# Kernel optimization log

Hardware: AMD Instinct MI355X
Metric: run time of the kernel (lower is better)

## Reference

```python
import jax, jax.numpy as jnp
import numpy as np

DEC_H = 1024
ENC_H_TOTAL = 1024  # enc_hid_size * enc_num_dirs


def setup_inputs() -> dict:
    key = jax.random.key(0)
    ks = jax.random.split(key, 10)
    N, L = 64, 1024
    s = 0.02
    return {
        "dec_h_curr": jax.random.normal(ks[0], (N, DEC_H), jnp.float32),
        "enc_hids": jax.random.normal(ks[1], (N, L, ENC_H_TOTAL), jnp.float32),
        # project_dec_hids: Linear(dec_H, dec_H)
        "W_dec": jax.random.normal(ks[2], (DEC_H, DEC_H), jnp.float32) * s,
        "b_dec": jnp.zeros((DEC_H,), jnp.float32),
        # project_enc_hids: Linear(enc_H*nDir, dec_H)
        "W_enc": jax.random.normal(ks[3], (ENC_H_TOTAL, DEC_H), jnp.float32) * s,
        "b_enc": jnp.zeros((DEC_H,), jnp.float32),
        # project_to_one_dim: Linear(dec_H, 1)
        "W_one": jax.random.normal(ks[4], (DEC_H, 1), jnp.float32) * s,
        "b_one": jnp.zeros((1,), jnp.float32),
        # project_att_hids: Linear(enc_H*nDir, dec_H)
        "W_att": jax.random.normal(ks[5], (ENC_H_TOTAL, DEC_H), jnp.float32) * s,
        "b_att": jnp.zeros((DEC_H,), jnp.float32),
    }


def reference(dec_h_curr, enc_hids, W_dec, b_dec, W_enc, b_enc, W_one, b_one, W_att, b_att):
    # additive (Bahdanau) attention branch
    d = dec_h_curr @ W_dec + b_dec                     # N x dec_H
    e = jnp.einsum('nle,ed->nld', enc_hids, W_enc) + b_enc  # N x L x dec_H
    scores = jnp.einsum('nld,do->nl', jnp.tanh(d[:, None, :] + e), W_one) + b_one[0]  # N x L
    alpha = jax.nn.softmax(scores, axis=-1)            # N x L
    ctx = jnp.einsum('nl,nle->ne', alpha, enc_hids)    # N x enc_H_total
    h_att_curr = ctx @ W_att + b_att                   # N x dec_H
    return h_att_curr, alpha
```

## Files before the change

kernel.cpp:

```cpp
#include <hip/hip_runtime.h>
#include <cstdio>
#include <cstdint>


typedef __bf16 bf16x8 __attribute__((ext_vector_type(8)));
typedef float f32x4 __attribute__((ext_vector_type(4)));
typedef unsigned short us8 __attribute__((ext_vector_type(8)));

static __device__ __forceinline__ unsigned short f2b(float f) {
  union { float f; unsigned u; } v; v.f = f;
  unsigned r = (v.u + 0x7fffu + ((v.u >> 16) & 1u)) >> 16;
  return (unsigned short)r;
}
static __device__ __forceinline__ float b2f(unsigned short u) {
  union { unsigned u; float f; } v; v.u = ((unsigned)u) << 16;
  return v.f;
}
static __device__ __forceinline__ void gl_lds16(const void* g, void* l) {
  __builtin_amdgcn_global_load_lds(
      (const __attribute__((address_space(1))) unsigned int*)g,
      (__attribute__((address_space(3))) unsigned int*)l, 16, 0, 0);
}
static __device__ __forceinline__ float fast_tanh(float x) {
  float ax = __builtin_fminf(__builtin_fabsf(x), 18.0f);
  float u = __builtin_amdgcn_exp2f(ax * 2.88539008177792681f);
  float t = (u - 1.0f) * __builtin_amdgcn_rcpf(u + 1.0f);
  return __builtin_copysignf(t, x);
}

__global__ __launch_bounds__(256) void prep_k(
    const float* __restrict__ enc, unsigned short* __restrict__ Ap,
    const float* __restrict__ W_enc, unsigned short* __restrict__ Bp,
    const float* __restrict__ dec_h, const float* __restrict__ W_dec,
    const float* __restrict__ b_dec, const float* __restrict__ b_enc,
    float* __restrict__ addterm) {
  __shared__ __align__(16) unsigned short tile[8192];
  const int bid = blockIdx.x;
  const int t = threadIdx.x;

  if (bid < 128) {
    const int Tn = bid >> 4, kt = bid & 15;
    #pragma unroll
    for (int it = 0; it < 8; ++it) {
      int idx = it * 256 + t;
      int kk = idx >> 5, n4 = idx & 31;
      const float4 v = *(const float4*)(W_enc + (size_t)(kt * 64 + kk) * 1024 + Tn * 128 + n4 * 4);
      int c = kk >> 3, j = kk & 7;
      #pragma unroll
      for (int x = 0; x < 4; ++x) {
        int mm = n4 * 4 + x;
        float fv = (x == 0) ? v.x : (x == 1) ? v.y : (x == 2) ? v.z : v.w;
        tile[(mm * 8 + (c ^ (mm & 7))) * 8 + j] = f2b(fv);
      }
    }
    __syncthreads();
    #pragma unroll
    for (int it = 0; it < 4; ++it) {
      int p = it * 256 + t;
      int c = p >> 7, m = p & 127;
      us8 v = *(const us8*)&tile[(m * 8 + (c ^ (m & 7))) * 8];
      *(us8*)(Bp + ((size_t)bid * 1024 + p) * 8) = v;
    }
  } else if (bid < 384) {
    const int bid2 = bid - 128;
    const int jb = bid2 & 3, n = bid2 >> 2;
    float* xs = (float*)tile;
    for (int i = t; i < 1024; i += 256) xs[i] = dec_h[n * 1024 + i];
    __syncthreads();
    int j = jb * 256 + t;
    float s = 0.f;
    #pragma unroll 8
    for (int k = 0; k < 1024; ++k) s += xs[k] * W_dec[(size_t)k * 1024 + j];
    addterm[n * 1024 + j] = s + b_dec[j] + b_enc[j];
  } else {
    const int ba = bid - 384;
    const int T = ba >> 4, kt = ba & 15;
    #pragma unroll
    for (int it = 0; it < 8; ++it) {
      int idx = it * 256 + t;
      int m = idx >> 4, c4 = idx & 15;
      const float4 v = *(const float4*)(enc + (size_t)(T * 128 + m) * 1024 + kt * 64 + c4 * 4);
      ushort4 o;
      o.x = f2b(v.x); o.y = f2b(v.y); o.z = f2b(v.z); o.w = f2b(v.w);
      int c = c4 >> 1, half = c4 & 1;
      *(ushort4*)&tile[(m * 8 + (c ^ (m & 7))) * 8 + half * 4] = o;
    }
    __syncthreads();
    #pragma unroll
    for (int it = 0; it < 4; ++it) {
      int p = it * 256 + t;
      int c = p >> 7, m = p & 127;
      us8 v = *(const us8*)&tile[(m * 8 + (c ^ (m & 7))) * 8];
      *(us8*)(Ap + ((size_t)ba * 1024 + p) * 8) = v;
    }
  }
}

__global__ __launch_bounds__(512, 2) void score_gemm(
    const unsigned short* __restrict__ Ap, const unsigned short* __restrict__ Bp,
    const float* __restrict__ addterm, const float* __restrict__ Wone,
    float* __restrict__ spart) {
  __shared__ __align__(16) unsigned short lA[32768];
  __shared__ __align__(16) unsigned short lB[32768];
  const int tid = threadIdx.x;
  const int lane = tid & 63, wave = tid >> 6;
  const int wm = wave >> 2, wn = wave & 3;
  const int q = lane >> 4, r = lane & 15;

  const int flat = blockIdx.x;
  const int tl = (flat & 7) * 128 + (flat >> 3);
  const int nb = tl & 3, mb = tl >> 2;

  f32x4 acc[8][4];
  #pragma unroll
  for (int i = 0; i < 8; ++i)
    #pragma unroll
    for (int j = 0; j < 4; ++j) acc[i][j] = (f32x4){0.f, 0.f, 0.f, 0.f};

  const unsigned short* gA0 = Ap + (((size_t)(2 * mb + 0) * 16) * 1024 + tid) * 8;
  const unsigned short* gA1 = Ap + (((size_t)(2 * mb + 1) * 16) * 1024 + tid) * 8;
  const unsigned short* gB0 = Bp + (((size_t)(2 * nb + 0) * 16) * 1024 + tid) * 8;
  const unsigned short* gB1 = Bp + (((size_t)(2 * nb + 1) * 16) * 1024 + tid) * 8;

  const unsigned short* rdA = &lA[(wm * 1024 + q * 128 + r) * 8];
  const unsigned short* rdB = &lB[((wn >> 1) * 1024 + q * 128 + (wn & 1) * 64 + r) * 8];

  bf16x8 af[4], bg[4];

#define SA(h, t, s) gl_lds16((h ? gA1 : gA0) + ((size_t)(t) * 1024 + (s) * 512) * 8, \
                             &lA[((((t) & 1) * 2048 + (h) * 1024 + (s) * 512 + wave * 64) * 8)])
#define SB(h, t, s) gl_lds16((h ? gB1 : gB0) + ((size_t)(t) * 1024 + (s) * 512) * 8, \
                             &lB[((((t) & 1) * 2048 + (h) * 1024 + (s) * 512 + wave * 64) * 8)])
#define RD_BG(b, s) { \
  bg[0] = *(const bf16x8*)&rdB[((b) * 2048 + (s) * 512 +  0) * 8]; \
  bg[1] = *(const bf16x8*)&rdB[((b) * 2048 + (s) * 512 + 16) * 8]; \
  bg[2] = *(const bf16x8*)&rdB[((b) * 2048 + (s) * 512 + 32) * 8]; \
  bg[3] = *(const bf16x8*)&rdB[((b) * 2048 + (s) * 512 + 48) * 8]; }
#define RD_AF(b, s, mh) { \
  af[0] = *(const bf16x8*)&rdA[((b) * 2048 + (s) * 512 + (mh) * 64 +  0) * 8]; \
  af[1] = *(const bf16x8*)&rdA[((b) * 2048 + (s) * 512 + (mh) * 64 + 16) * 8]; \
  af[2] = *(const bf16x8*)&rdA[((b) * 2048 + (s) * 512 + (mh) * 64 + 32) * 8]; \
  af[3] = *(const bf16x8*)&rdA[((b) * 2048 + (s) * 512 + (mh) * 64 + 48) * 8]; }
#define MMA_CORE(mh) \
  __builtin_amdgcn_s_barrier(); \
  asm volatile("s_waitcnt lgkmcnt(0)" ::: "memory"); \
  __builtin_amdgcn_s_setprio(1); \
  acc[(mh)*4+0][0] = __builtin_amdgcn_mfma_f32_16x16x32_bf16(af[0], bg[0], acc[(mh)*4+0][0], 0, 0, 0); \
  acc[(mh)*4+0][1] = __builtin_amdgcn_mfma_f32_16x16x32_bf16(af[0], bg[1], acc[(mh)*4+0][1], 0, 0, 0); \
  acc[(mh)*4+0][2] = __builtin_amdgcn_mfma_f32_16x16x32_bf16(af[0], bg[2], acc[(mh)*4+0][2], 0, 0, 0); \
  acc[(mh)*4+0][3] = __builtin_amdgcn_mfma_f32_16x16x32_bf16(af[0], bg[3], acc[(mh)*4+0][3], 0, 0, 0); \
  acc[(mh)*4+1][0] = __builtin_amdgcn_mfma_f32_16x16x32_bf16(af[1], bg[0], acc[(mh)*4+1][0], 0, 0, 0); \
  acc[(mh)*4+1][1] = __builtin_amdgcn_mfma_f32_16x16x32_bf16(af[1], bg[1], acc[(mh)*4+1][1], 0, 0, 0); \
  acc[(mh)*4+1][2] = __builtin_amdgcn_mfma_f32_16x16x32_bf16(af[1], bg[2], acc[(mh)*4+1][2], 0, 0, 0); \
  acc[(mh)*4+1][3] = __builtin_amdgcn_mfma_f32_16x16x32_bf16(af[1], bg[3], acc[(mh)*4+1][3], 0, 0, 0); \
  acc[(mh)*4+2][0] = __builtin_amdgcn_mfma_f32_16x16x32_bf16(af[2], bg[0], acc[(mh)*4+2][0], 0, 0, 0); \
  acc[(mh)*4+2][1] = __builtin_amdgcn_mfma_f32_16x16x32_bf16(af[2], bg[1], acc[(mh)*4+2][1], 0, 0, 0); \
  acc[(mh)*4+2][2] = __builtin_amdgcn_mfma_f32_16x16x32_bf16(af[2], bg[2], acc[(mh)*4+2][2], 0, 0, 0); \
  acc[(mh)*4+2][3] = __builtin_amdgcn_mfma_f32_16x16x32_bf16(af[2], bg[3], acc[(mh)*4+2][3], 0, 0, 0); \
  acc[(mh)*4+3][0] = __builtin_amdgcn_mfma_f32_16x16x32_bf16(af[3], bg[0], acc[(mh)*4+3][0], 0, 0, 0); \
  acc[(mh)*4+3][1] = __builtin_amdgcn_mfma_f32_16x16x32_bf16(af[3], bg[1], acc[(mh)*4+3][1], 0, 0, 0); \
  acc[(mh)*4+3][2] = __builtin_amdgcn_mfma_f32_16x16x32_bf16(af[3], bg[2], acc[(mh)*4+3][2], 0, 0, 0); \
  acc[(mh)*4+3][3] = __builtin_amdgcn_mfma_f32_16x16x32_bf16(af[3], bg[3], acc[(mh)*4+3][3], 0, 0, 0); \
  __builtin_amdgcn_s_setprio(0);
#define BAR __builtin_amdgcn_s_barrier()
#define VM4 asm volatile("s_waitcnt vmcnt(4)" ::: "memory")
#define VM0 asm volatile("s_waitcnt vmcnt(0)" ::: "memory")

  SA(0, 0, 0); SA(1, 0, 0); SB(0, 0, 0); SB(1, 0, 0);
  SA(0, 0, 1); SA(1, 0, 1); SB(0, 0, 1); SB(1, 0, 1);
  SA(0, 1, 0); SA(1, 1, 0); SB(0, 1, 0); SB(1, 1, 0);
  VM4;
  BAR;

  #pragma unroll 1
  for (int it = 0; it < 7; ++it) {
    const int t1 = 2 * it + 1, t2 = 2 * it + 2, t3 = 2 * it + 3;
    RD_BG(0, 0); RD_AF(0, 0, 0); SA(0, t1, 1); SA(1, t1, 1); MMA_CORE(0); BAR;
    RD_AF(0, 0, 1); SB(0, t1, 1); SB(1, t1, 1); MMA_CORE(1); BAR;
    RD_BG(0, 1); RD_AF(0, 1, 0); SA(0, t2, 0); SA(1, t2, 0); MMA_CORE(0); BAR;
    RD_AF(0, 1, 1); SB(0, t2, 0); SB(1, t2, 0); MMA_CORE(1); VM4; BAR;
    RD_BG(1, 0); RD_AF(1, 0, 0); SA(0, t2, 1); SA(1, t2, 1); MMA_CORE(0); BAR;
    RD_AF(1, 0, 1); SB(0, t2, 1); SB(1, t2, 1); MMA_CORE(1); BAR;
    RD_BG(1, 1); RD_AF(1, 1, 0); SA(0, t3, 0); SA(1, t3, 0); MMA_CORE(0); BAR;
    RD_AF(1, 1, 1); SB(0, t3, 0); SB(1, t3, 0); MMA_CORE(1); VM4; BAR;
  }

  RD_BG(0, 0); RD_AF(0, 0, 0); SA(0, 15, 1); SA(1, 15, 1); MMA_CORE(0); BAR;
  RD_AF(0, 0, 1); SB(0, 15, 1); SB(1, 15, 1); MMA_CORE(1); BAR;
  RD_BG(0, 1); RD_AF(0, 1, 0); MMA_CORE(0); BAR;
  RD_AF(0, 1, 1); MMA_CORE(1); VM0; BAR;
  RD_BG(1, 0); RD_AF(1, 0, 0); MMA_CORE(0); BAR;
  RD_AF(1, 0, 1); MMA_CORE(1); BAR;
  RD_BG(1, 1); RD_AF(1, 1, 0); MMA_CORE(0); BAR;
  RD_AF(1, 1, 1); MMA_CORE(1);

#undef SA
#undef SB
#undef RD_BG
#undef RD_AF
#undef MMA_CORE
#undef BAR
#undef VM4
#undef VM0

  const int nrow = mb >> 2;
  float addv[4], wv[4];
  #pragma unroll
  for (int ni = 0; ni < 4; ++ni) {
    int col = nb * 256 + wn * 64 + ni * 16 + r;
    addv[ni] = addterm[nrow * 1024 + col];
    wv[ni] = Wone[col];
  }
  #pragma unroll
  for (int mi = 0; mi < 8; ++mi) {
    #pragma unroll
    for (int rr = 0; rr < 4; ++rr) {
      float s = 0.f;
      #pragma unroll
      for (int ni = 0; ni < 4; ++ni)
        s += fast_tanh(acc[mi][ni][rr] + addv[ni]) * wv[ni];
      s += __shfl_xor(s, 1);
      s += __shfl_xor(s, 2);
      s += __shfl_xor(s, 4);
      s += __shfl_xor(s, 8);
      if (r == 0) {
        size_t row = (size_t)mb * 256 + wm * 128 + mi * 16 + q * 4 + rr;
        spart[row * 16 + nb * 4 + wn] = s;
      }
    }
  }
}

__global__ __launch_bounds__(256) void ctx_fused(
    const float* __restrict__ spart, float* __restrict__ alpha,
    const unsigned short* __restrict__ Ap, float* __restrict__ ctx) {
  const int kt = blockIdx.x, n = blockIdx.y, t = threadIdx.x;
  __shared__ float red[8];
  __shared__ float al[1024];

  float sv[4];
  #pragma unroll
  for (int i = 0; i < 4; ++i) {
    int l = i * 256 + t;
    const float4* p = (const float4*)(spart + ((size_t)n * 1024 + l) * 16);
    float4 v0 = p[0], v1 = p[1], v2 = p[2], v3 = p[3];
    sv[i] = (v0.x + v0.y + v0.z + v0.w) + (v1.x + v1.y + v1.z + v1.w) +
            (v2.x + v2.y + v2.z + v2.w) + (v3.x + v3.y + v3.z + v3.w);
  }
  float m = fmaxf(fmaxf(sv[0], sv[1]), fmaxf(sv[2], sv[3]));
  for (int o = 32; o > 0; o >>= 1) m = fmaxf(m, __shfl_xor(m, o));
  if ((t & 63) == 0) red[t >> 6] = m;
  __syncthreads();
  float gm = fmaxf(fmaxf(red[0], red[1]), fmaxf(red[2], red[3]));
  float e[4], s = 0.f;
  #pragma unroll
  for (int i = 0; i < 4; ++i) { e[i] = expf(sv[i] - gm); s += e[i]; }
  for (int o = 32; o > 0; o >>= 1) s += __shfl_xor(s, o);
  if ((t & 63) == 0) red[4 + (t >> 6)] = s;
  __syncthreads();
  float inv = 1.0f / (red[4] + red[5] + red[6] + red[7]);
  #pragma unroll
  for (int i = 0; i < 4; ++i) {
    float a = e[i] * inv;
    al[i * 256 + t] = a;
    if (kt == 0) alpha[(size_t)n * 1024 + i * 256 + t] = a;
  }
  __syncthreads();

  const int c = t >> 5, ls = t & 31;
  float acc[8] = {0.f, 0.f, 0.f, 0.f, 0.f, 0.f, 0.f, 0.f};
  #pragma unroll 4
  for (int lb = 0; lb < 32; ++lb) {
    int l = lb * 32 + ls;
    int M = n * 1024 + l;
    int T = M >> 7, mm = M & 127;
    us8 v = *(const us8*)(Ap + ((((size_t)T * 16 + kt) * 8 + c) * 128 + mm) * 8);
    float w = al[l];
    #pragma unroll
    for (int j = 0; j < 8; ++j) acc[j] += w * b2f(v[j]);
  }
  #pragma unroll
  for (int off = 1; off <= 16; off <<= 1)
    #pragma unroll
    for (int j = 0; j < 8; ++j) acc[j] += __shfl_xor(acc[j], off);
  if (ls == 0) {
    #pragma unroll
    for (int j = 0; j < 8; ++j) ctx[(size_t)n * 1024 + kt * 64 + c * 8 + j] = acc[j];
  }
}

__global__ __launch_bounds__(256) void hatt_k(
    const float* __restrict__ ctx, const float* __restrict__ W_att,
    const float* __restrict__ b_att, float* __restrict__ out) {
  __shared__ float cs[1024];
  __shared__ float red[4][64];
  const int n = blockIdx.y;
  const int jb = blockIdx.x;
  const int t = threadIdx.x;
  for (int i = t; i < 1024; i += 256) cs[i] = ctx[(size_t)n * 1024 + i];
  __syncthreads();
  const int j = jb * 64 + (t & 63);
  const int ks = t >> 6;
  float s = 0.f;
  const float* Wp = W_att + (size_t)(ks * 256) * 1024 + j;
  #pragma unroll 8
  for (int k = 0; k < 256; ++k) s += cs[ks * 256 + k] * Wp[(size_t)k * 1024];
  red[ks][t & 63] = s;
  __syncthreads();
  if (t < 64) {
    out[(size_t)n * 1024 + jb * 64 + t] =
        red[0][t] + red[1][t] + red[2][t] + red[3][t] + b_att[jb * 64 + t];
  }
}

extern "C" void kernel_launch(void* const* d_in, const int* in_sizes, int n_in,
                              void* d_out, int out_size, void* d_ws, size_t ws_size,
                              hipStream_t stream) {
  const float* dec_h = (const float*)d_in[0];
  const float* enc   = (const float*)d_in[1];
  const float* W_dec = (const float*)d_in[2];
  const float* b_dec = (const float*)d_in[3];
  const float* W_enc = (const float*)d_in[4];
  const float* b_enc = (const float*)d_in[5];
  const float* W_one = (const float*)d_in[6];
  const float* W_att = (const float*)d_in[8];
  const float* b_att = (const float*)d_in[9];
  float* out = (float*)d_out;

  char* ws = (char*)d_ws;
  const size_t OFF_A   = 0;
  const size_t OFF_B   = 134217728;
  const size_t OFF_ADD = OFF_B + 2097152;
  const size_t OFF_SP  = OFF_ADD + 262144;
  const size_t OFF_CTX = OFF_SP + 4194304;
  const size_t NEED    = OFF_CTX + 262144;
  if (ws_size < NEED) {
    fprintf(stderr, "kernel_launch: ws too small (%zu < %zu)\n", ws_size, NEED);
    return;
  }
  unsigned short* Ap = (unsigned short*)(ws + OFF_A);
  unsigned short* Bp = (unsigned short*)(ws + OFF_B);
  float* addterm = (float*)(ws + OFF_ADD);
  float* spart   = (float*)(ws + OFF_SP);
  float* ctx     = (float*)(ws + OFF_CTX);
  float* alpha   = out + 65536;

  prep_k<<<8576, 256, 0, stream>>>(enc, Ap, W_enc, Bp, dec_h, W_dec, b_dec, b_enc, addterm);
  score_gemm<<<1024, 512, 0, stream>>>(Ap, Bp, addterm, W_one, spart);
  ctx_fused<<<dim3(16, 64), 256, 0, stream>>>(spart, alpha, Ap, ctx);
  hatt_k<<<dim3(16, 64), 256, 0, stream>>>(ctx, W_att, b_att, out);
}
```

Before: 642.0 us.

## Deepen GEMM LDS pipeline to four-stage ring with prefetch distance three

Restructures the main bf16 MFMA GEMM loop from a two-buffer, half-tile staging scheme into a four-slot LDS ring buffer where each K-step is a single 32-wide slice, loaded three steps ahead. Waits use vmcnt(8) so more global-to-LDS loads stay in flight while MFMAs run, hiding memory latency better. A sched_barrier is added after the LDS wait so the compiler cannot move MFMAs ahead of it. The cost is more outstanding loads and a more intricate epilogue drain sequence.

Result: no change. 631.7 us (-1.6%).

```diff
diff --git a/kernel.cpp b/kernel.cpp
--- a/kernel.cpp
+++ b/kernel.cpp
@@ -117,33 +117,34 @@
     #pragma unroll
     for (int j = 0; j < 4; ++j) acc[i][j] = (f32x4){0.f, 0.f, 0.f, 0.f};
 
-  const unsigned short* gA0 = Ap + (((size_t)(2 * mb + 0) * 16) * 1024 + tid) * 8;
-  const unsigned short* gA1 = Ap + (((size_t)(2 * mb + 1) * 16) * 1024 + tid) * 8;
-  const unsigned short* gB0 = Bp + (((size_t)(2 * nb + 0) * 16) * 1024 + tid) * 8;
-  const unsigned short* gB1 = Bp + (((size_t)(2 * nb + 1) * 16) * 1024 + tid) * 8;
-
-  const unsigned short* rdA = &lA[(wm * 1024 + q * 128 + r) * 8];
-  const unsigned short* rdB = &lB[((wn >> 1) * 1024 + q * 128 + (wn & 1) * 64 + r) * 8];
+  const unsigned short* pA0 = Ap + (((size_t)(2 * mb + 0) * 16384) + tid) * 8;
+  const unsigned short* pA1 = Ap + (((size_t)(2 * mb + 1) * 16384) + tid) * 8;
+  const unsigned short* pB0 = Bp + (((size_t)(2 * nb + 0) * 16384) + tid) * 8;
+  const unsigned short* pB1 = Bp + (((size_t)(2 * nb + 1) * 16384) + tid) * 8;
+
+  const unsigned short* rdA = &lA[(wm * 512 + q * 128 + r) * 8];
+  const unsigned short* rdB = &lB[((wn >> 1) * 512 + q * 128 + (wn & 1) * 64 + r) * 8];
 
   bf16x8 af[4], bg[4];
 
-#define SA(h, t, s) gl_lds16((h ? gA1 : gA0) + ((size_t)(t) * 1024 + (s) * 512) * 8, \
-                             &lA[((((t) & 1) * 2048 + (h) * 1024 + (s) * 512 + wave * 64) * 8)])
-#define SB(h, t, s) gl_lds16((h ? gB1 : gB0) + ((size_t)(t) * 1024 + (s) * 512) * 8, \
-                             &lB[((((t) & 1) * 2048 + (h) * 1024 + (s) * 512 + wave * 64) * 8)])
-#define RD_BG(b, s) { \
-  bg[0] = *(const bf16x8*)&rdB[((b) * 2048 + (s) * 512 +  0) * 8]; \
-  bg[1] = *(const bf16x8*)&rdB[((b) * 2048 + (s) * 512 + 16) * 8]; \
-  bg[2] = *(const bf16x8*)&rdB[((b) * 2048 + (s) * 512 + 32) * 8]; \
-  bg[3] = *(const bf16x8*)&rdB[((b) * 2048 + (s) * 512 + 48) * 8]; }
-#define RD_AF(b, s, mh) { \
-  af[0] = *(const bf16x8*)&rdA[((b) * 2048 + (s) * 512 + (mh) * 64 +  0) * 8]; \
-  af[1] = *(const bf16x8*)&rdA[((b) * 2048 + (s) * 512 + (mh) * 64 + 16) * 8]; \
-  af[2] = *(const bf16x8*)&rdA[((b) * 2048 + (s) * 512 + (mh) * 64 + 32) * 8]; \
-  af[3] = *(const bf16x8*)&rdA[((b) * 2048 + (s) * 512 + (mh) * 64 + 48) * 8]; }
+#define SA(h, off, u) gl_lds16(((h) ? pA1 : pA0) + (size_t)(off) * 4096, \
+                               &lA[(((u) * 1024 + (h) * 512 + wave * 64) * 8)])
+#define SB(h, off, u) gl_lds16(((h) ? pB1 : pB0) + (size_t)(off) * 4096, \
+                               &lB[(((u) * 1024 + (h) * 512 + wave * 64) * 8)])
+#define RD_BG(u) { \
+  bg[0] = *(const bf16x8*)&rdB[((u) * 1024 +  0) * 8]; \
+  bg[1] = *(const bf16x8*)&rdB[((u) * 1024 + 16) * 8]; \
+  bg[2] = *(const bf16x8*)&rdB[((u) * 1024 + 32) * 8]; \
+  bg[3] = *(const bf16x8*)&rdB[((u) * 1024 + 48) * 8]; }
+#define RD_AF(u, mh) { \
+  af[0] = *(const bf16x8*)&rdA[((u) * 1024 + (mh) * 64 +  0) * 8]; \
+  af[1] = *(const bf16x8*)&rdA[((u) * 1024 + (mh) * 64 + 16) * 8]; \
+  af[2] = *(const bf16x8*)&rdA[((u) * 1024 + (mh) * 64 + 32) * 8]; \
+  af[3] = *(const bf16x8*)&rdA[((u) * 1024 + (mh) * 64 + 48) * 8]; }
 #define MMA_CORE(mh) \
   __builtin_amdgcn_s_barrier(); \
   asm volatile("s_waitcnt lgkmcnt(0)" ::: "memory"); \
+  __builtin_amdgcn_sched_barrier(0); \
   __builtin_amdgcn_s_setprio(1); \
   acc[(mh)*4+0][0] = __builtin_amdgcn_mfma_f32_16x16x32_bf16(af[0], bg[0], acc[(mh)*4+0][0], 0, 0, 0); \
   acc[(mh)*4+0][1] = __builtin_amdgcn_mfma_f32_16x16x32_bf16(af[0], bg[1], acc[(mh)*4+0][1], 0, 0, 0); \
@@ -163,36 +164,37 @@
   acc[(mh)*4+3][3] = __builtin_amdgcn_mfma_f32_16x16x32_bf16(af[3], bg[3], acc[(mh)*4+3][3], 0, 0, 0); \
   __builtin_amdgcn_s_setprio(0);
 #define BAR __builtin_amdgcn_s_barrier()
+#define VM8 asm volatile("s_waitcnt vmcnt(8)" ::: "memory")
 #define VM4 asm volatile("s_waitcnt vmcnt(4)" ::: "memory")
 #define VM0 asm volatile("s_waitcnt vmcnt(0)" ::: "memory")
 
   SA(0, 0, 0); SA(1, 0, 0); SB(0, 0, 0); SB(1, 0, 0);
-  SA(0, 0, 1); SA(1, 0, 1); SB(0, 0, 1); SB(1, 0, 1);
-  SA(0, 1, 0); SA(1, 1, 0); SB(0, 1, 0); SB(1, 1, 0);
-  VM4;
+  SA(0, 1, 1); SA(1, 1, 1); SB(0, 1, 1); SB(1, 1, 1);
+  SA(0, 2, 2); SA(1, 2, 2); SB(0, 2, 2); SB(1, 2, 2);
+  VM8;
   BAR;
 
   #pragma unroll 1
-  for (int it = 0; it < 7; ++it) {
-    const int t1 = 2 * it + 1, t2 = 2 * it + 2, t3 = 2 * it + 3;
-    RD_BG(0, 0); RD_AF(0, 0, 0); SA(0, t1, 1); SA(1, t1, 1); MMA_CORE(0); BAR;
-    RD_AF(0, 0, 1); SB(0, t1, 1); SB(1, t1, 1); MMA_CORE(1); BAR;
-    RD_BG(0, 1); RD_AF(0, 1, 0); SA(0, t2, 0); SA(1, t2, 0); MMA_CORE(0); BAR;
-    RD_AF(0, 1, 1); SB(0, t2, 0); SB(1, t2, 0); MMA_CORE(1); VM4; BAR;
-    RD_BG(1, 0); RD_AF(1, 0, 0); SA(0, t2, 1); SA(1, t2, 1); MMA_CORE(0); BAR;
-    RD_AF(1, 0, 1); SB(0, t2, 1); SB(1, t2, 1); MMA_CORE(1); BAR;
-    RD_BG(1, 1); RD_AF(1, 1, 0); SA(0, t3, 0); SA(1, t3, 0); MMA_CORE(0); BAR;
-    RD_AF(1, 1, 1); SB(0, t3, 0); SB(1, t3, 0); MMA_CORE(1); VM4; BAR;
-  }
-
-  RD_BG(0, 0); RD_AF(0, 0, 0); SA(0, 15, 1); SA(1, 15, 1); MMA_CORE(0); BAR;
-  RD_AF(0, 0, 1); SB(0, 15, 1); SB(1, 15, 1); MMA_CORE(1); BAR;
-  RD_BG(0, 1); RD_AF(0, 1, 0); MMA_CORE(0); BAR;
-  RD_AF(0, 1, 1); MMA_CORE(1); VM0; BAR;
-  RD_BG(1, 0); RD_AF(1, 0, 0); MMA_CORE(0); BAR;
-  RD_AF(1, 0, 1); MMA_CORE(1); BAR;
-  RD_BG(1, 1); RD_AF(1, 1, 0); MMA_CORE(0); BAR;
-  RD_AF(1, 1, 1); MMA_CORE(1);
+  for (int it2 = 0; it2 < 7; ++it2) {
+    RD_BG(0); RD_AF(0, 0); SA(0, 3, 3); SA(1, 3, 3); MMA_CORE(0); BAR;
+    RD_AF(0, 1);           SB(0, 3, 3); SB(1, 3, 3); MMA_CORE(1); VM8; BAR;
+    RD_BG(1); RD_AF(1, 0); SA(0, 4, 0); SA(1, 4, 0); MMA_CORE(0); BAR;
+    RD_AF(1, 1);           SB(0, 4, 0); SB(1, 4, 0); MMA_CORE(1); VM8; BAR;
+    RD_BG(2); RD_AF(2, 0); SA(0, 5, 1); SA(1, 5, 1); MMA_CORE(0); BAR;
+    RD_AF(2, 1);           SB(0, 5, 1); SB(1, 5, 1); MMA_CORE(1); VM8; BAR;
+    RD_BG(3); RD_AF(3, 0); SA(0, 6, 2); SA(1, 6, 2); MMA_CORE(0); BAR;
+    RD_AF(3, 1);           SB(0, 6, 2); SB(1, 6, 2); MMA_CORE(1); VM8; BAR;
+    pA0 += 4 * 4096; pA1 += 4 * 4096; pB0 += 4 * 4096; pB1 += 4 * 4096;
+  }
+
+  RD_BG(0); RD_AF(0, 0); SA(0, 3, 3); SA(1, 3, 3); MMA_CORE(0); BAR;
+  RD_AF(0, 1);           SB(0, 3, 3); SB(1, 3, 3); MMA_CORE(1); VM8; BAR;
+  RD_BG(1); RD_AF(1, 0); MMA_CORE(0); BAR;
+  RD_AF(1, 1);           MMA_CORE(1); VM4; BAR;
+  RD_BG(2); RD_AF(2, 0); MMA_CORE(0); BAR;
+  RD_AF(2, 1);           MMA_CORE(1); VM0; BAR;
+  RD_BG(3); RD_AF(3, 0); MMA_CORE(0); BAR;
+  RD_AF(3, 1);           MMA_CORE(1);
 
 #undef SA
 #undef SB
@@ -200,6 +202,7 @@
 #undef RD_AF
 #undef MMA_CORE
 #undef BAR
+#undef VM8
 #undef VM4
 #undef VM0
 
```
